# Kernel tuning notes

Hardware: AMD Instinct MI355X
Metric: run time of the kernel (lower is better)

## Reference

```python
import jax, jax.numpy as jnp
import numpy as np

FREQ_DIM = 64
BLOCK_DIM = 64
N = 256          # lattice sites
CH = 6           # channel_num -> block diagonals at offsets -1, 0, +1
S = 2 * 16 + CH - 2   # seq_num = 36
BS = 4           # block_size (kron of two 2x2 matrices)
HID = 128
EPS = 1e-5
B = 32

_e = np.eye(2)
_sx = np.array([[0., 1.], [1., 0.]])
_siy = np.array([[0., 1.], [-1., 0.]])
_sz = np.array([[1., 0.], [0., -1.]])
_p = [_e, _sx, _siy, _sz]
KRONS = jnp.asarray(np.stack([np.kron(_p[a], _p[b]) for a in range(4) for b in range(4)]).astype(np.float32))  # (16,4,4)
Z1 = KRONS[12]  # kron(sigma_z, I) used for interaction blocks ('z1')


def _bn(h, g, b):
    # BatchNorm1d in training mode: biased batch statistics over axis 0
    mu = h.mean(axis=0)
    v = h.var(axis=0)
    return g * (h - mu) / jnp.sqrt(v + EPS) + b


def _mlp(x, Win, bin_, Wmid, bmid, Wout, bout, gamma, beta):
    # depth-4 MLP: Lin+ReLU, then (BN,Lin,ReLU) x2, then BN,Lin,ReLU
    h = jax.nn.relu(x @ Win + bin_)
    for i in range(Wmid.shape[0]):
        h = jax.nn.relu(_bn(h, gamma[i], beta[i]) @ Wmid[i] + bmid[i])
    return jax.nn.relu(_bn(h, gamma[-1], beta[-1]) @ Wout + bout)


def _lstm(xs, h0, c0, Wih, Whh, bih, bhh):
    # xs: (B, T, S); torch gate order i, f, g, o
    def step(carry, x_t):
        h, c = carry
        gates = x_t @ Wih.T + h @ Whh.T + (bih + bhh)
        i, f, g, o = jnp.split(gates, 4, axis=-1)
        c = jax.nn.sigmoid(f) * c + jax.nn.sigmoid(i) * jnp.tanh(g)
        h = jax.nn.sigmoid(o) * jnp.tanh(c)
        return (h, c), h
    _, hs = jax.lax.scan(step, (h0, c0), jnp.swapaxes(xs, 0, 1))
    return jnp.swapaxes(hs, 0, 1)


def setup_inputs() -> dict:
    key = jax.random.key(0)
    ks = iter(jax.random.split(key, 48))
    def w(shape, s=0.05):
        return jax.random.normal(next(ks), shape, dtype=jnp.float32) * s
    d = {
        'x': w((B, FREQ_DIM + BLOCK_DIM), 1.0),
        'fd_Win': w((FREQ_DIM, HID)), 'fd_bin': w((HID,)),
        'fd_Wmid': w((2, HID, HID)), 'fd_bmid': w((2, HID)),
        'fd_Wout': w((HID, S)), 'fd_bout': w((S,)),
        'fd_gamma': jnp.ones((3, HID), jnp.float32), 'fd_beta': jnp.zeros((3, HID), jnp.float32),
        'bd_Win': w((BLOCK_DIM, HID)), 'bd_bin': w((HID,)),
        'bd_Wmid': w((2, HID, HID)), 'bd_bmid': w((2, HID)),
        'bd_Wout': w((HID, S)), 'bd_bout': w((S,)),
        'bd_gamma': jnp.ones((3, HID), jnp.float32), 'bd_beta': jnp.zeros((3, HID), jnp.float32),
        'sc_Win': w((S, 1, HID)), 'sc_bin': w((S, HID)),
        'sc_Wmid': w((S, 2, HID, HID)), 'sc_bmid': w((S, 2, HID)),
        'sc_Wout': w((S, HID, N)), 'sc_bout': w((S, N)),
        'sc_gamma': jnp.ones((S, 3, HID), jnp.float32), 'sc_beta': jnp.zeros((S, 3, HID), jnp.float32),
        'lstm_Wih': w((4 * S, S)), 'lstm_Whh': w((4 * S, S)),
        'lstm_bih': w((4 * S,)), 'lstm_bhh': w((4 * S,)),
        'mix_W': w((S, 2 * S)), 'mix_b': w((S,)),
    }
    return d


def reference(x, fd_Win, fd_bin, fd_Wmid, fd_bmid, fd_Wout, fd_bout, fd_gamma, fd_beta,
              bd_Win, bd_bin, bd_Wmid, bd_bmid, bd_Wout, bd_bout, bd_gamma, bd_beta,
              sc_Win, sc_bin, sc_Wmid, sc_bmid, sc_Wout, sc_bout, sc_gamma, sc_beta,
              lstm_Wih, lstm_Whh, lstm_bih, lstm_bhh, mix_W, mix_b):
    Bsz = x.shape[0]
    block = _mlp(x[:, FREQ_DIM:], bd_Win, bd_bin, bd_Wmid, bd_bmid, bd_Wout, bd_bout, bd_gamma, bd_beta)  # (B,S)
    freq = _mlp(x[:, :FREQ_DIM], fd_Win, fd_bin, fd_Wmid, fd_bmid, fd_Wout, fd_bout, fd_gamma, fd_beta)   # (B,S)
    # S independent scalar->N MLPs, batched with vmap over the stacked params
    sc = jax.vmap(_mlp)(freq.T[:, :, None], sc_Win, sc_bin, sc_Wmid, sc_bmid,
                        sc_Wout, sc_bout, sc_gamma, sc_beta)  # (S,B,N)
    freq_seq = jnp.cos(sc).transpose(1, 2, 0)   # (B,N,S)
    seq = _lstm(freq_seq, block, jnp.zeros_like(block), lstm_Wih, lstm_Whh, lstm_bih, lstm_bhh)  # (B,N,S)
    block_seq = jnp.concatenate([jnp.broadcast_to(block[:, :, None], (Bsz, S, N)),
                                 jnp.swapaxes(seq, 1, 2)], axis=1)  # (B,2S,N)
    # 1x1 Conv2d == channel mixing matmul
    mixed = jnp.einsum('bcn,oc->bon', block_seq, mix_W) + mix_b[None, :, None]  # (B,S,N)
    inter = mixed[:, :CH - 2]                          # (B,CH-2,N)
    onsite = mixed[:, CH - 2:].reshape(Bsz, 2, 16, N)  # (B,2,16,N)
    H_int = jnp.einsum('bcn,ij->bcnij', inter, Z1)         # (B,CH-2,N,4,4)
    H_os = jnp.einsum('bgkn,kij->bgnij', onsite, KRONS)    # (B,2,N,4,4) summed over 16 pairs
    half = (CH - 2) // 2
    strips = jnp.concatenate([H_int[:, :half], H_os, H_int[:, half:]], axis=1)  # (B,CH,N,4,4)
    strips = strips.reshape(Bsz, CH // 2, 2, N, BS, BS)
    # banded block assembly: strip i lives on block-diagonal offset i - (CH//2)//2
    grid = jnp.zeros((Bsz, 2, N, N, BS, BS), dtype=x.dtype)
    for i in range(CH // 2):
        o = i - (CH // 2) // 2
        rows = jnp.arange(N - abs(o)) + max(0, -o)
        cols = rows + o
        grid = grid.at[:, :, rows, cols].set(strips[:, i][:, :, rows])
    matrix = grid.transpose(0, 1, 2, 4, 3, 5).reshape(Bsz, 2, N * BS, N * BS)
    return matrix
```

## Files before the change

kernel.cpp:

```cpp
#include <hip/hip_runtime.h>
#include <math.h>

#define EPSF 1e-5f
typedef __attribute__((ext_vector_type(2))) float f32x2;
typedef __attribute__((ext_vector_type(4))) float f32x4;

__device__ __forceinline__ float sigf(float x) { return 1.f / (1.f + __expf(-x)); }
__device__ __forceinline__ float tanhf_fast(float x) { return 1.f - 2.f / (__expf(2.f * x) + 1.f); }

__device__ __forceinline__ float pauliv(int p, int r, int c) {
    switch (p) {
        case 0: return (r == c) ? 1.f : 0.f;
        case 1: return (r != c) ? 1.f : 0.f;
        case 2: return (r == 0 && c == 1) ? 1.f : ((r == 1 && c == 0) ? -1.f : 0.f);
        default: return (r == c) ? ((r == 0) ? 1.f : -1.f) : 0.f;
    }
}

__device__ void mlp64_body(const float* __restrict__ xin,
                           const float* __restrict__ Win,
                           const float* __restrict__ bin_,
                           const float* __restrict__ Wmid,
                           const float* __restrict__ bmid,
                           const float* __restrict__ Wout,
                           const float* __restrict__ bout,
                           const float* __restrict__ gamma,
                           const float* __restrict__ beta,
                           float* __restrict__ out)
{
    __shared__ float sX[2048];
    __shared__ float sA[4096];
    __shared__ float sB[4096];
    __shared__ float sMu[128], sRs[128];
    int tid = threadIdx.x;

    for (int idx = tid; idx < 2048; idx += 1024) {
        int b = idx >> 6, c = idx & 63;
        sX[idx] = xin[b * 128 + c];
    }
    __syncthreads();

    for (int idx = tid; idx < 4096; idx += 1024) {
        int b = idx >> 7, j = idx & 127;
        float acc = bin_[j];
        for (int c = 0; c < 64; ++c) acc = fmaf(sX[b * 64 + c], Win[c * 128 + j], acc);
        sA[idx] = fmaxf(acc, 0.f);
    }
    __syncthreads();

    float* cur = sA;
    float* nxt = sB;
    for (int l = 0; l < 3; ++l) {
        if (tid < 128) {
            float s = 0.f, s2 = 0.f;
            for (int b = 0; b < 32; ++b) {
                float v = cur[b * 128 + tid];
                s += v; s2 += v * v;
            }
            float mu = s * (1.f / 32.f);
            float var = s2 * (1.f / 32.f) - mu * mu;
            sMu[tid] = mu;
            sRs[tid] = rsqrtf(var + EPSF);
        }
        __syncthreads();
        for (int idx = tid; idx < 4096; idx += 1024) {
            int j = idx & 127;
            cur[idx] = gamma[l * 128 + j] * (cur[idx] - sMu[j]) * sRs[j] + beta[l * 128 + j];
        }
        __syncthreads();
        if (l < 2) {
            for (int idx = tid; idx < 4096; idx += 1024) {
                int b = idx >> 7, j = idx & 127;
                float acc = bmid[l * 128 + j];
                for (int c = 0; c < 128; ++c)
                    acc = fmaf(cur[b * 128 + c], Wmid[(l * 128 + c) * 128 + j], acc);
                nxt[idx] = fmaxf(acc, 0.f);
            }
            __syncthreads();
            float* t = cur; cur = nxt; nxt = t;
        } else {
            for (int idx = tid; idx < 1152; idx += 1024) {
                int b = idx / 36, j = idx - b * 36;
                float acc = bout[j];
                for (int c = 0; c < 128; ++c)
                    acc = fmaf(cur[b * 128 + c], Wout[c * 36 + j], acc);
                out[idx] = fmaxf(acc, 0.f);
            }
        }
    }
}

__global__ __launch_bounds__(1024) void k_mlp2(
    const float* __restrict__ x,
    const float* fdWin, const float* fdbin, const float* fdWmid, const float* fdbmid,
    const float* fdWout, const float* fdbout, const float* fdg, const float* fdbt,
    const float* bdWin, const float* bdbin, const float* bdWmid, const float* bdbmid,
    const float* bdWout, const float* bdbout, const float* bdg, const float* bdbt,
    float* freq, float* blk)
{
    if (blockIdx.x == 0)
        mlp64_body(x + 64, bdWin, bdbin, bdWmid, bdbmid, bdWout, bdbout, bdg, bdbt, blk);
    else
        mlp64_body(x, fdWin, fdbin, fdWmid, fdbmid, fdWout, fdbout, fdg, fdbt, freq);
}

__global__ __launch_bounds__(512) void k_sc1(
    const float* __restrict__ freq,
    const float* __restrict__ Win,
    const float* __restrict__ bin_,
    const float* __restrict__ Wmid,
    const float* __restrict__ bmid,
    const float* __restrict__ gamma,
    const float* __restrict__ beta,
    float* __restrict__ actW)
{
    int s = blockIdx.x, tid = threadIdx.x;
    __shared__ float sA[4096];
    __shared__ float sB[4096];
    __shared__ float sMu[128], sRs[128];
    const float* Wm = Wmid + (size_t)s * 2 * 128 * 128;
    const float* gm = gamma + s * 3 * 128;
    const float* bt = beta + s * 3 * 128;

    for (int idx = tid; idx < 4096; idx += 512) {
        int b = idx >> 7, j = idx & 127;
        float acc = fmaf(freq[b * 36 + s], Win[s * 128 + j], bin_[s * 128 + j]);
        sA[idx] = fmaxf(acc, 0.f);
    }
    __syncthreads();

    float* cur = sA;
    float* nxt = sB;
    for (int l = 0; l < 3; ++l) {
        if (tid < 128) {
            float sm = 0.f, s2 = 0.f;
            for (int b = 0; b < 32; ++b) {
                float v = cur[b * 128 + tid];
                sm += v; s2 += v * v;
            }
            float mu = sm * (1.f / 32.f);
            float var = s2 * (1.f / 32.f) - mu * mu;
            sMu[tid] = mu;
            sRs[tid] = rsqrtf(var + EPSF);
        }
        __syncthreads();
        for (int idx = tid; idx < 4096; idx += 512) {
            int j = idx & 127;
            cur[idx] = gm[l * 128 + j] * (cur[idx] - sMu[j]) * sRs[j] + bt[l * 128 + j];
        }
        __syncthreads();
        if (l < 2) {
            int jj = tid & 127, bb = tid >> 7;
            float acc[8];
            #pragma unroll
            for (int k = 0; k < 8; ++k) acc[k] = bmid[(s * 2 + l) * 128 + jj];
            for (int c = 0; c < 128; ++c) {
                float w = Wm[(l * 128 + c) * 128 + jj];
                #pragma unroll
                for (int k = 0; k < 8; ++k)
                    acc[k] = fmaf(cur[(bb + 4 * k) * 128 + c], w, acc[k]);
            }
            __syncthreads();
            #pragma unroll
            for (int k = 0; k < 8; ++k) nxt[(bb + 4 * k) * 128 + jj] = fmaxf(acc[k], 0.f);
            __syncthreads();
            float* t = cur; cur = nxt; nxt = t;
        } else {
            for (int idx = tid; idx < 4096; idx += 512)
                actW[(size_t)s * 4096 + idx] = cur[idx];
        }
    }
}

__global__ __launch_bounds__(512) void k_sc2(
    const float* __restrict__ actW,
    const float* __restrict__ Wout,
    const float* __restrict__ bout,
    float* __restrict__ fseq2)
{
    int bidx = blockIdx.x;
    int s = bidx >> 2, q = bidx & 3;
    int tid = threadIdx.x;
    __shared__ float sAct[4096];
    for (int idx = tid; idx < 4096; idx += 512)
        sAct[idx] = actW[(size_t)s * 4096 + idx];
    __syncthreads();

    int nn = (tid & 63) + q * 64;
    int bb = tid >> 6;
    const float* Wo = Wout + (size_t)s * 128 * 256;
    float acc[4];
    #pragma unroll
    for (int k = 0; k < 4; ++k) acc[k] = bout[s * 256 + nn];
    #pragma unroll 4
    for (int c = 0; c < 128; ++c) {
        float w = Wo[c * 256 + nn];
        #pragma unroll
        for (int k = 0; k < 4; ++k)
            acc[k] = fmaf(sAct[(bb + 8 * k) * 128 + c], w, acc[k]);
    }
    #pragma unroll
    for (int k = 0; k < 4; ++k) {
        float v = fmaxf(acc[k], 0.f);
        fseq2[((size_t)s * 32 + bb + 8 * k) * 256 + nn] = __cosf(v);
    }
}

__global__ __launch_bounds__(512) void k_xg(
    const float* __restrict__ fseq2, const float* __restrict__ Wih,
    const float* __restrict__ bih, const float* __restrict__ bhh,
    float* __restrict__ Xg)
{
    int t = blockIdx.x, tid = threadIdx.x;
    __shared__ float sF[1152];
    __shared__ float sWt[36 * 144];
    for (int idx = tid; idx < 1152; idx += 512) {
        int s = idx >> 5, b = idx & 31;
        sF[b * 36 + s] = fseq2[(size_t)idx * 256 + t];
    }
    for (int idx = tid; idx < 5184; idx += 512) {
        int j = idx / 36, s = idx - j * 36;
        sWt[s * 144 + j] = Wih[idx];
    }
    __syncthreads();
    for (int idx = tid; idx < 4608; idx += 512) {
        int b = idx / 144, j = idx - b * 144;
        int g = j / 36, u = j - g * 36;
        float acc = bih[j] + bhh[j];
        #pragma unroll
        for (int s = 0; s < 36; ++s)
            acc = fmaf(sF[b * 36 + s], sWt[s * 144 + j], acc);
        Xg[(((size_t)b * 256 + t) * 36 + u) * 4 + g] = acc;
    }
}

#define PF 8
__global__ __launch_bounds__(128) void k_lstm(
    const float* __restrict__ Xg,
    const float* __restrict__ blk,
    const float* __restrict__ Whh,
    float* __restrict__ hseq2)
{
    __shared__ f32x2 sGO[40];
    __shared__ float sH[40];

    int b = blockIdx.x;
    int wid = threadIdx.x >> 6;
    int lane = threadIdx.x & 63;
    int uu = lane < 36 ? lane : 35;
    bool active = lane < 36;

    f32x2 w2[36];
    {
        const float* wA = Whh + (size_t)(wid * 72 + uu) * 36;
        const float* wB = Whh + (size_t)(wid * 72 + 36 + uu) * 36;
        #pragma unroll
        for (int k = 0; k < 36; ++k) w2[k] = f32x2{wA[k], wB[k]};
    }

    float hv = blk[b * 36 + uu];
    float c = 0.f;
    const f32x2* xb2 = (const f32x2*)(Xg + (size_t)b * 256 * 144);
    float* hout = hseq2 + (size_t)b * 256 * 36;

    f32x2 pipe[PF];
    #pragma unroll
    for (int i = 0; i < PF; ++i) pipe[i] = xb2[(i * 36 + uu) * 2 + wid];

    #pragma unroll 8
    for (int t = 0; t < 256; ++t) {
        f32x2 a0 = pipe[t & (PF - 1)];
        if (t + PF < 256) pipe[t & (PF - 1)] = xb2[((t + PF) * 36 + uu) * 2 + wid];

        f32x2 a1 = f32x2{0.f, 0.f};
        #pragma unroll
        for (int k = 0; k < 36; k += 2) {
            float h0 = __int_as_float(__builtin_amdgcn_readlane(__float_as_int(hv), k));
            float h1 = __int_as_float(__builtin_amdgcn_readlane(__float_as_int(hv), k + 1));
            a0 = __builtin_elementwise_fma(w2[k], f32x2{h0, h0}, a0);
            a1 = __builtin_elementwise_fma(w2[k + 1], f32x2{h1, h1}, a1);
        }
        a0 += a1;

        if (wid == 1 && active) {
            float gv = tanhf_fast(a0.x);
            float ov = sigf(a0.y);
            sGO[uu] = f32x2{gv, ov};
        }
        __syncthreads();
        if (wid == 0 && active) {
            float iv = sigf(a0.x);
            float fv = sigf(a0.y);
            f32x2 go = sGO[uu];
            c = fmaf(fv, c, iv * go.x);
            float hn = go.y * tanhf_fast(c);
            hv = hn;
            sH[uu] = hn;
            hout[t * 36 + uu] = hn;
        }
        __syncthreads();
        if (wid == 1) hv = sH[uu];
    }
}

__global__ __launch_bounds__(256) void k_mixed(
    const float* __restrict__ blk, const float* __restrict__ hseq2,
    const float* __restrict__ mixW, const float* __restrict__ mixb,
    float* __restrict__ mixed)
{
    int bq = blockIdx.x;
    int b = bq >> 2, oq = bq & 3;
    int tid = threadIdx.x;
    __shared__ float sH[256 * 37];
    __shared__ float sW[9 * 36];
    __shared__ float sBase[9];
    for (int idx = tid; idx < 9216; idx += 256) {
        int t = idx / 36, u = idx - t * 36;
        sH[t * 37 + u] = hseq2[(size_t)b * 9216 + idx];
    }
    for (int idx = tid; idx < 9 * 36; idx += 256) {
        int o = idx / 36, u = idx - o * 36;
        sW[idx] = mixW[(oq * 9 + o) * 72 + 36 + u];
    }
    if (tid < 9) {
        int o = oq * 9 + tid;
        float acc = mixb[o];
        for (int c = 0; c < 36; ++c) acc = fmaf(mixW[o * 72 + c], blk[b * 36 + c], acc);
        sBase[tid] = acc;
    }
    __syncthreads();
    int n = tid;
    #pragma unroll
    for (int o = 0; o < 9; ++o) {
        float acc = sBase[o];
        #pragma unroll
        for (int u = 0; u < 36; ++u)
            acc = fmaf(sW[o * 36 + u], sH[n * 37 + u], acc);
        mixed[((size_t)b * 36 + oq * 9 + o) * 256 + n] = acc;
    }
}

__global__ __launch_bounds__(256) void k_out(
    const float* __restrict__ mixed, float* __restrict__ out)
{
    int bid = blockIdx.x;
    int bg = bid >> 5, chunk = bid & 31;
    int g = bg & 1, b = bg >> 1;
    float* base = out + (size_t)bg * (1024 * 1024);
    f32x4* rp = (f32x4*)(base + (size_t)chunk * 32 * 1024);
    f32x4 z = f32x4{0.f, 0.f, 0.f, 0.f};
    #pragma unroll
    for (int i = 0; i < 32; ++i)
        rp[i * 256 + threadIdx.x] = z;
    __syncthreads();

    int tid = threadIdx.x;
    if (tid < 8) {
        int n = chunk * 8 + tid;
        const float* mb = mixed + (size_t)b * 36 * 256;
        float vSub = mb[(size_t)g * 256 + n];
        float vSup = mb[(size_t)(2 + g) * 256 + n];
        float ch[16];
        #pragma unroll
        for (int k = 0; k < 16; ++k) ch[k] = mb[(size_t)(4 + 16 * g + k) * 256 + n];
        float d[16];
        #pragma unroll
        for (int e = 0; e < 16; ++e) {
            int r = e >> 2, cc = e & 3;
            float acc = 0.f;
            #pragma unroll
            for (int k = 0; k < 16; ++k) {
                float kv = pauliv(k >> 2, r >> 1, cc >> 1) * pauliv(k & 3, r & 1, cc & 1);
                if (kv == 1.f) acc = acc + ch[k];
                else if (kv == -1.f) acc = acc - ch[k];
            }
            d[e] = acc;
        }
        #pragma unroll
        for (int r = 0; r < 4; ++r)
            *(f32x4*)(base + (size_t)(4 * n + r) * 1024 + 4 * n) =
                f32x4{d[r * 4 + 0], d[r * 4 + 1], d[r * 4 + 2], d[r * 4 + 3]};
        if (n > 0) {
            #pragma unroll
            for (int r = 0; r < 4; ++r)
                base[(size_t)(4 * n + r) * 1024 + 4 * (n - 1) + r] = (r < 2) ? vSub : -vSub;
        }
        if (n < 255) {
            #pragma unroll
            for (int r = 0; r < 4; ++r)
                base[(size_t)(4 * n + r) * 1024 + 4 * (n + 1) + r] = (r < 2) ? vSup : -vSup;
        }
    }
}

extern "C" void kernel_launch(void* const* d_in, const int* in_sizes, int n_in,
                              void* d_out, int out_size, void* d_ws, size_t ws_size,
                              hipStream_t stream) {
    const float* x      = (const float*)d_in[0];
    const float* fdWin  = (const float*)d_in[1];
    const float* fdbin  = (const float*)d_in[2];
    const float* fdWmid = (const float*)d_in[3];
    const float* fdbmid = (const float*)d_in[4];
    const float* fdWout = (const float*)d_in[5];
    const float* fdbout = (const float*)d_in[6];
    const float* fdg    = (const float*)d_in[7];
    const float* fdbt   = (const float*)d_in[8];
    const float* bdWin  = (const float*)d_in[9];
    const float* bdbin  = (const float*)d_in[10];
    const float* bdWmid = (const float*)d_in[11];
    const float* bdbmid = (const float*)d_in[12];
    const float* bdWout = (const float*)d_in[13];
    const float* bdbout = (const float*)d_in[14];
    const float* bdg    = (const float*)d_in[15];
    const float* bdbt   = (const float*)d_in[16];
    const float* scWin  = (const float*)d_in[17];
    const float* scbin  = (const float*)d_in[18];
    const float* scWmid = (const float*)d_in[19];
    const float* scbmid = (const float*)d_in[20];
    const float* scWout = (const float*)d_in[21];
    const float* scbout = (const float*)d_in[22];
    const float* scg    = (const float*)d_in[23];
    const float* scbt   = (const float*)d_in[24];
    const float* Wih    = (const float*)d_in[25];
    const float* Whh    = (const float*)d_in[26];
    const float* bih    = (const float*)d_in[27];
    const float* bhh    = (const float*)d_in[28];
    const float* mixW   = (const float*)d_in[29];
    const float* mixb   = (const float*)d_in[30];

    float* ws    = (float*)d_ws;
    float* freq  = ws;
    float* blk   = ws + 1152;
    float* fseq2 = ws + 2304;
    float* Xg    = ws + 297216;
    float* hseq2 = ws + 1476864;
    float* mixed = ws + 1771776;
    float* actW  = Xg;

    float* out = (float*)d_out;

    k_mlp2<<<2, 1024, 0, stream>>>(x,
        fdWin, fdbin, fdWmid, fdbmid, fdWout, fdbout, fdg, fdbt,
        bdWin, bdbin, bdWmid, bdbmid, bdWout, bdbout, bdg, bdbt,
        freq, blk);
    k_sc1<<<36, 512, 0, stream>>>(freq, scWin, scbin, scWmid, scbmid, scg, scbt, actW);
    k_sc2<<<144, 512, 0, stream>>>(actW, scWout, scbout, fseq2);
    k_xg<<<256, 512, 0, stream>>>(fseq2, Wih, bih, bhh, Xg);
    k_lstm<<<32, 128, 0, stream>>>(Xg, blk, Whh, hseq2);
    k_mixed<<<128, 256, 0, stream>>>(blk, hseq2, mixW, mixb, mixed);
    k_out<<<2048, 256, 0, stream>>>(mixed, out);
}
```

Before: 356.8 us.

## Overlap output zero-fill with LSTM recurrence and halve LSTM barriers

The large output zero-fill moves out of the final scatter kernel and into extra blocks of the LSTM launch, so the bandwidth-bound fill runs alongside the latency-bound recurrence. The LSTM step now has both waves compute their gate activations and swap them through double-buffered shared memory, giving one barrier per timestep instead of two. The hidden-state matvec also uses four accumulators instead of two for more instruction-level parallelism. The output kernel then only writes the banded blocks, with one thread per site. Risks: the fill blocks may compete with the LSTM blocks for memory bandwidth and scheduling, and the fill length depends on out_size being a byte count.

```diff
diff --git a/kernel.cpp b/kernel.cpp
--- a/kernel.cpp
+++ b/kernel.cpp
@@ -7,6 +7,9 @@
 
 __device__ __forceinline__ float sigf(float x) { return 1.f / (1.f + __expf(-x)); }
 __device__ __forceinline__ float tanhf_fast(float x) { return 1.f - 2.f / (__expf(2.f * x) + 1.f); }
+__device__ __forceinline__ float rdlane(float v, int k) {
+    return __int_as_float(__builtin_amdgcn_readlane(__float_as_int(v), k));
+}
 
 __device__ __forceinline__ float pauliv(int p, int r, int c) {
     switch (p) {
@@ -235,15 +238,24 @@
 }
 
 #define PF 8
-__global__ __launch_bounds__(128) void k_lstm(
+#define NZBLK 4032
+__global__ __launch_bounds__(128) void k_lstm_zero(
     const float* __restrict__ Xg,
     const float* __restrict__ blk,
     const float* __restrict__ Whh,
-    float* __restrict__ hseq2)
-{
-    __shared__ f32x2 sGO[40];
-    __shared__ float sH[40];
-
+    float* __restrict__ hseq2,
+    float* __restrict__ out, long total4)
+{
+    if (blockIdx.x >= 32) {
+        f32x4* o = (f32x4*)out;
+        f32x4 z = f32x4{0.f, 0.f, 0.f, 0.f};
+        long start = (long)(blockIdx.x - 32) * 128 + threadIdx.x;
+        long stride = (long)NZBLK * 128;
+        for (long i = start; i < total4; i += stride) o[i] = z;
+        return;
+    }
+
+    __shared__ f32x2 sEx[2][2][40];
     int b = blockIdx.x;
     int wid = threadIdx.x >> 6;
     int lane = threadIdx.x & 63;
@@ -269,37 +281,32 @@
 
     #pragma unroll 8
     for (int t = 0; t < 256; ++t) {
-        f32x2 a0 = pipe[t & (PF - 1)];
+        f32x2 acc0 = pipe[t & (PF - 1)];
         if (t + PF < 256) pipe[t & (PF - 1)] = xb2[((t + PF) * 36 + uu) * 2 + wid];
 
-        f32x2 a1 = f32x2{0.f, 0.f};
-        #pragma unroll
-        for (int k = 0; k < 36; k += 2) {
-            float h0 = __int_as_float(__builtin_amdgcn_readlane(__float_as_int(hv), k));
-            float h1 = __int_as_float(__builtin_amdgcn_readlane(__float_as_int(hv), k + 1));
-            a0 = __builtin_elementwise_fma(w2[k], f32x2{h0, h0}, a0);
-            a1 = __builtin_elementwise_fma(w2[k + 1], f32x2{h1, h1}, a1);
-        }
-        a0 += a1;
-
-        if (wid == 1 && active) {
-            float gv = tanhf_fast(a0.x);
-            float ov = sigf(a0.y);
-            sGO[uu] = f32x2{gv, ov};
-        }
+        f32x2 acc1 = f32x2{0.f, 0.f}, acc2 = f32x2{0.f, 0.f}, acc3 = f32x2{0.f, 0.f};
+        #pragma unroll
+        for (int k = 0; k < 36; k += 4) {
+            float h0 = rdlane(hv, k),     h1 = rdlane(hv, k + 1);
+            float h2 = rdlane(hv, k + 2), h3 = rdlane(hv, k + 3);
+            acc0 = __builtin_elementwise_fma(w2[k],     f32x2{h0, h0}, acc0);
+            acc1 = __builtin_elementwise_fma(w2[k + 1], f32x2{h1, h1}, acc1);
+            acc2 = __builtin_elementwise_fma(w2[k + 2], f32x2{h2, h2}, acc2);
+            acc3 = __builtin_elementwise_fma(w2[k + 3], f32x2{h3, h3}, acc3);
+        }
+        f32x2 a = (acc0 + acc1) + (acc2 + acc3);
+
+        f32x2 mypair;
+        if (wid == 0) mypair = f32x2{sigf(a.x), sigf(a.y)};
+        else          mypair = f32x2{tanhf_fast(a.x), sigf(a.y)};
+        if (active) sEx[t & 1][wid][uu] = mypair;
         __syncthreads();
-        if (wid == 0 && active) {
-            float iv = sigf(a0.x);
-            float fv = sigf(a0.y);
-            f32x2 go = sGO[uu];
-            c = fmaf(fv, c, iv * go.x);
-            float hn = go.y * tanhf_fast(c);
-            hv = hn;
-            sH[uu] = hn;
-            hout[t * 36 + uu] = hn;
-        }
-        __syncthreads();
-        if (wid == 1) hv = sH[uu];
+        f32x2 other = sEx[t & 1][wid ^ 1][uu];
+        f32x2 ivfv = (wid == 0) ? mypair : other;
+        f32x2 gvov = (wid == 0) ? other : mypair;
+        c = fmaf(ivfv.y, c, ivfv.x * gvov.x);
+        hv = gvov.y * tanhf_fast(c);
+        if (wid == 0 && active) hout[t * 36 + uu] = hv;
     }
 }
 
@@ -340,56 +347,46 @@
     }
 }
 
-__global__ __launch_bounds__(256) void k_out(
+__global__ __launch_bounds__(256) void k_sparse(
     const float* __restrict__ mixed, float* __restrict__ out)
 {
-    int bid = blockIdx.x;
-    int bg = bid >> 5, chunk = bid & 31;
+    int bg = blockIdx.x;
     int g = bg & 1, b = bg >> 1;
-    float* base = out + (size_t)bg * (1024 * 1024);
-    f32x4* rp = (f32x4*)(base + (size_t)chunk * 32 * 1024);
-    f32x4 z = f32x4{0.f, 0.f, 0.f, 0.f};
-    #pragma unroll
-    for (int i = 0; i < 32; ++i)
-        rp[i * 256 + threadIdx.x] = z;
-    __syncthreads();
-
-    int tid = threadIdx.x;
-    if (tid < 8) {
-        int n = chunk * 8 + tid;
-        const float* mb = mixed + (size_t)b * 36 * 256;
-        float vSub = mb[(size_t)g * 256 + n];
-        float vSup = mb[(size_t)(2 + g) * 256 + n];
-        float ch[16];
-        #pragma unroll
-        for (int k = 0; k < 16; ++k) ch[k] = mb[(size_t)(4 + 16 * g + k) * 256 + n];
-        float d[16];
-        #pragma unroll
-        for (int e = 0; e < 16; ++e) {
-            int r = e >> 2, cc = e & 3;
-            float acc = 0.f;
-            #pragma unroll
-            for (int k = 0; k < 16; ++k) {
-                float kv = pauliv(k >> 2, r >> 1, cc >> 1) * pauliv(k & 3, r & 1, cc & 1);
-                if (kv == 1.f) acc = acc + ch[k];
-                else if (kv == -1.f) acc = acc - ch[k];
-            }
-            d[e] = acc;
-        }
+    int n = threadIdx.x;
+    const float* mb = mixed + (size_t)b * 36 * 256;
+    float vSub = mb[(size_t)g * 256 + n];
+    float vSup = mb[(size_t)(2 + g) * 256 + n];
+    float ch[16];
+    #pragma unroll
+    for (int k = 0; k < 16; ++k) ch[k] = mb[(size_t)(4 + 16 * g + k) * 256 + n];
+    float d[16];
+    #pragma unroll
+    for (int e = 0; e < 16; ++e) {
+        int r = e >> 2, cc = e & 3;
+        float acc = 0.f;
+        #pragma unroll
+        for (int k = 0; k < 16; ++k) {
+            float kv = pauliv(k >> 2, r >> 1, cc >> 1) * pauliv(k & 3, r & 1, cc & 1);
+            if (kv == 1.f) acc = acc + ch[k];
+            else if (kv == -1.f) acc = acc - ch[k];
+        }
+        d[e] = acc;
+    }
+
+    float* base = out + (size_t)bg * 1024 * 1024;
+    #pragma unroll
+    for (int r = 0; r < 4; ++r)
+        *(f32x4*)(base + (size_t)(4 * n + r) * 1024 + 4 * n) =
+            f32x4{d[r * 4 + 0], d[r * 4 + 1], d[r * 4 + 2], d[r * 4 + 3]};
+    if (n > 0) {
         #pragma unroll
         for (int r = 0; r < 4; ++r)
-            *(f32x4*)(base + (size_t)(4 * n + r) * 1024 + 4 * n) =
-                f32x4{d[r * 4 + 0], d[r * 4 + 1], d[r * 4 + 2], d[r * 4 + 3]};
-        if (n > 0) {
-            #pragma unroll
-            for (int r = 0; r < 4; ++r)
-                base[(size_t)(4 * n + r) * 1024 + 4 * (n - 1) + r] = (r < 2) ? vSub : -vSub;
-        }
-        if (n < 255) {
-            #pragma unroll
-            for (int r = 0; r < 4; ++r)
-                base[(size_t)(4 * n + r) * 1024 + 4 * (n + 1) + r] = (r < 2) ? vSup : -vSup;
-        }
+            base[(size_t)(4 * n + r) * 1024 + 4 * (n - 1) + r] = (r < 2) ? vSub : -vSub;
+    }
+    if (n < 255) {
+        #pragma unroll
+        for (int r = 0; r < 4; ++r)
+            base[(size_t)(4 * n + r) * 1024 + 4 * (n + 1) + r] = (r < 2) ? vSup : -vSup;
     }
 }
 
@@ -438,6 +435,7 @@
     float* actW  = Xg;
 
     float* out = (float*)d_out;
+    long total4 = (long)out_size / 4;
 
     k_mlp2<<<2, 1024, 0, stream>>>(x,
         fdWin, fdbin, fdWmid, fdbmid, fdWout, fdbout, fdg, fdbt,
@@ -446,7 +444,7 @@
     k_sc1<<<36, 512, 0, stream>>>(freq, scWin, scbin, scWmid, scbmid, scg, scbt, actW);
     k_sc2<<<144, 512, 0, stream>>>(actW, scWout, scbout, fseq2);
     k_xg<<<256, 512, 0, stream>>>(fseq2, Wih, bih, bhh, Xg);
-    k_lstm<<<32, 128, 0, stream>>>(Xg, blk, Whh, hseq2);
+    k_lstm_zero<<<32 + NZBLK, 128, 0, stream>>>(Xg, blk, Whh, hseq2, out, total4);
     k_mixed<<<128, 256, 0, stream>>>(blk, hseq2, mixW, mixb, mixed);
-    k_out<<<2048, 256, 0, stream>>>(mixed, out);
-}
+    k_sparse<<<64, 256, 0, stream>>>(mixed, out);
+}
```

New measurement: 326.2 us. -8.6%, faster.
